# Optimization experiments

Measured on AMD Instinct MI355X. Metric: run time of the kernel, lower is better.

## Reference

```python
import jax, jax.numpy as jnp
import numpy as np

SEM_DIM = 512
SEM_SIZE = 2048
N_LEVELS = 9           # acoustic FSQ levels
HALF = (N_LEVELS - 1) / 2.0
EPS = 1e-5


def setup_inputs() -> dict:
    key = jax.random.key(0)
    k1, k2, k3, k4, k5, k6 = jax.random.split(key, 6)
    B, T, ACO_DIM = 16, 4096, 32
    return {
        "x": jax.random.normal(k1, (B, SEM_DIM + ACO_DIM, T), dtype=jnp.float32),
        "embedding_sum": jax.random.normal(k2, (SEM_SIZE, SEM_DIM), dtype=jnp.float32),
        "cluster_usage": jax.random.uniform(k3, (SEM_SIZE,), dtype=jnp.float32),
        "noise": jax.random.uniform(k4, (B, ACO_DIM, T), dtype=jnp.float32),
        "probs_sem": jax.random.uniform(k5, (B,), dtype=jnp.float32),
        "probs_aco": jax.random.uniform(k6, (B,), dtype=jnp.float32),
    }


def reference(x, embedding_sum, cluster_usage, noise, probs_sem, probs_aco):
    sem_in = x[:, :SEM_DIM, :]          # [B, 512, T]
    aco_in = x[:, SEM_DIM:, :]          # [B, 32, T]
    B, D, T = sem_in.shape

    # ---- semantic VQ path (cdist + argmin + embedding lookup + STE) ----
    emb = embedding_sum / jnp.clip(cluster_usage, EPS, None)[:, None]  # [K, D]
    xf = sem_in.transpose(0, 2, 1).reshape(B * T, D)                   # (b t) d
    # squared euclidean distance (argmin identical to cdist p=2 argmin)
    d2 = (jnp.sum(xf * xf, axis=1, keepdims=True)
          - 2.0 * (xf @ emb.T)
          + jnp.sum(emb * emb, axis=1))                                # [BT, K]
    sem_codes = jnp.argmin(d2, axis=-1).reshape(B, 1, T)               # [B,1,T]
    sem_quant = emb[sem_codes[:, 0, :]].transpose(0, 2, 1)             # b d t
    sem_mask = (probs_sem < 0.5)[:, None, None]
    sem_ste = sem_in + jax.lax.stop_gradient(sem_quant - sem_in)
    sem_out = jnp.where(sem_mask, sem_ste, sem_in)

    # ---- acoustic FSQ path with 50/25/25 stochastic routing ----
    z_b = jnp.tanh(aco_in) * HALF
    z_q = z_b + jax.lax.stop_gradient(jnp.round(z_b) - z_b)            # round STE
    noise_s = (noise * 2.0 - 1.0) * (1.0 / N_LEVELS) * HALF            # U[-s, s]*half
    z_dither = jnp.clip(z_b + noise_s, -HALF, HALF)
    qm = (probs_aco < 0.5)[:, None, None]
    dm = ((probs_aco >= 0.5) & (probs_aco < 0.75))[:, None, None]
    z_out = jnp.where(qm, z_q, jnp.where(dm, z_dither, z_b))
    aco_codes = jnp.clip(jnp.round(z_out + HALF), 0, N_LEVELS - 1).astype(jnp.int32)
    z_norm = z_out / HALF

    quantized = jnp.concatenate([sem_out, z_norm], axis=1)             # [B,544,T]
    codes = jnp.concatenate([sem_codes.astype(jnp.int32), aco_codes], axis=1)
    return quantized, codes
```

## Files before the change

kernel.cpp:

```cpp
#include <hip/hip_runtime.h>
#include <math.h>
#include <stdint.h>

typedef _Float16 f16;
typedef _Float16 f16x8 __attribute__((ext_vector_type(8)));
typedef float f32x4 __attribute__((ext_vector_type(4)));

#define B_    16
#define T_    4096
#define SEM   512
#define ACO   32
#define XROWS 544
#define CODES 2048
#define EPSC  1e-5f
#define HALFC 4.0f
#define ECLAMP 60000.0f


__global__ void bias_kernel(const float* __restrict__ esum,
                            const float* __restrict__ usage,
                            float* __restrict__ bias) {
    int c = blockIdx.x;
    float u = fmaxf(usage[c], EPSC);
    float s = 0.f;
    for (int d = threadIdx.x; d < SEM; d += 64) {
        float v = esum[(size_t)c * SEM + d] / u;
        s += v * v;
    }
    for (int off = 32; off; off >>= 1) s += __shfl_down(s, off);
    if (threadIdx.x == 0) bias[c] = 0.5f * s;
}

__global__ void embT_kernel(const float* __restrict__ esum,
                            const float* __restrict__ usage,
                            float* __restrict__ embT) {
    __shared__ float tile[32][33];
    int c0 = blockIdx.x * 32;
    int d0 = blockIdx.y * 32;
    int col = threadIdx.x & 31, r = threadIdx.x >> 5;
    for (int i = r; i < 32; i += 8) {
        float u = fmaxf(usage[c0 + i], EPSC);
        tile[col][i] = esum[(size_t)(c0 + i) * SEM + d0 + col] / u;
    }
    __syncthreads();
    for (int i = r; i < 32; i += 8)
        embT[(size_t)(d0 + i) * CODES + c0 + col] = tile[i][col];
}

__global__ void esplit_kernel(const float* __restrict__ esum,
                              const float* __restrict__ usage,
                              f16* __restrict__ EhT, f16* __restrict__ ElT) {
    int c = blockIdx.x;
    float u = fmaxf(usage[c], EPSC);
    for (int d = threadIdx.x; d < SEM; d += 256) {
        float e = esum[(size_t)c * SEM + d] / u;
        e = fminf(fmaxf(e, -ECLAMP), ECLAMP);
        f16 h = (f16)e;
        EhT[(size_t)c * SEM + d] = h;
        ElT[(size_t)c * SEM + d] = (f16)(e - (float)h);
    }
}

__global__ void xsplit_kernel(const float* __restrict__ x,
                              f16* __restrict__ XhT, f16* __restrict__ XlT) {
    int m0 = blockIdx.x * 256;
    int d0 = blockIdx.y * 32;
    int b  = m0 >> 12;
    int t  = (m0 & 4095) + (int)threadIdx.x;
    const float* xp = x + ((size_t)b * XROWS + d0) * T_ + t;
    int m = m0 + (int)threadIdx.x;

    f16x8 hv[4], lv[4];
#pragma unroll
    for (int j = 0; j < 4; j++) {
#pragma unroll
        for (int e = 0; e < 8; e++) {
            float v = xp[(size_t)(j * 8 + e) * T_];
            f16 h = (f16)v;
            hv[j][e] = h;
            lv[j][e] = (f16)(v - (float)h);
        }
    }
    f16* oh = XhT + (size_t)m * SEM + d0;
    f16* ol = XlT + (size_t)m * SEM + d0;
#pragma unroll
    for (int j = 0; j < 4; j++) {
        *(f16x8*)(oh + j * 8) = hv[j];
        *(f16x8*)(ol + j * 8) = lv[j];
    }
}

#define MB 256
#define NQ 512
#define NC 128
#define BK 32

__device__ __forceinline__ void gl_lds16(const f16* g, f16* l) {
    __builtin_amdgcn_global_load_lds(
        (const __attribute__((address_space(1))) unsigned int*)(g),
        (__attribute__((address_space(3))) unsigned int*)(l),
        16, 0, 0);
}

__global__ __launch_bounds__(256, 2) void argmin_mfma(
        const f16* __restrict__ XhT, const f16* __restrict__ XlT,
        const f16* __restrict__ EhT, const f16* __restrict__ ElT,
        const float* __restrict__ bias,
        float* __restrict__ pScore, int* __restrict__ pIdx) {
    __shared__ __align__(16) f16 Xh[MB * BK];
    __shared__ __align__(16) f16 Xl[MB * BK];
    __shared__ __align__(16) f16 Eh[NC * BK];
    __shared__ __align__(16) f16 El[NC * BK];

    int tid = threadIdx.x;
    int w   = tid >> 6;
    int l   = tid & 63;
    int q   = l >> 4;
    int r16 = l & 15;

    int m0      = blockIdx.x * MB;
    int quarter = blockIdx.y;

    int aoff = (w * 64 + r16) * BK + q * 8;
    int boff = r16 * BK + q * 8;

    float bestS[16];
    int   bestI[16];
#pragma unroll
    for (int i = 0; i < 16; i++) { bestS[i] = -3.4e38f; bestI[i] = 0; }

    for (int nc = 0; nc < 4; nc++) {
        int nbase = quarter * NQ + nc * NC;
        float bb[8];
#pragma unroll
        for (int ni = 0; ni < 8; ni++) bb[ni] = bias[nbase + ni * 16 + r16];

        f32x4 acc[4][8];
#pragma unroll
        for (int mi = 0; mi < 4; mi++)
#pragma unroll
            for (int ni = 0; ni < 8; ni++)
                acc[mi][ni] = (f32x4){0.f, 0.f, 0.f, 0.f};

        for (int k0 = 0; k0 < SEM; k0 += BK) {
            __syncthreads();
#pragma unroll
            for (int ii = 0; ii < 4; ii++) {
                int off16 = ii * 256 + tid;
                int mm = off16 >> 2, ch = off16 & 3;
                int gsrc = (m0 + mm) * SEM + k0 + ch * 8;
                gl_lds16(XhT + gsrc, Xh + off16 * 8);
                gl_lds16(XlT + gsrc, Xl + off16 * 8);
            }
#pragma unroll
            for (int ii = 0; ii < 2; ii++) {
                int off16 = ii * 256 + tid;
                int nn = off16 >> 2, ch = off16 & 3;
                int gsrc = (nbase + nn) * SEM + k0 + ch * 8;
                gl_lds16(EhT + gsrc, Eh + off16 * 8);
                gl_lds16(ElT + gsrc, El + off16 * 8);
            }
            __syncthreads();

            f16x8 ah[4], al[4];
#pragma unroll
            for (int mi = 0; mi < 4; mi++) {
                ah[mi] = *(const f16x8*)&Xh[aoff + mi * 16 * BK];
                al[mi] = *(const f16x8*)&Xl[aoff + mi * 16 * BK];
            }
#pragma unroll
            for (int ni = 0; ni < 8; ni++) {
                f16x8 bh = *(const f16x8*)&Eh[boff + ni * 16 * BK];
                f16x8 bl = *(const f16x8*)&El[boff + ni * 16 * BK];
#pragma unroll
                for (int mi = 0; mi < 4; mi++) {
                    f32x4 a0 = acc[mi][ni];
                    a0 = __builtin_amdgcn_mfma_f32_16x16x32_f16(al[mi], bh, a0, 0, 0, 0);
                    a0 = __builtin_amdgcn_mfma_f32_16x16x32_f16(ah[mi], bl, a0, 0, 0, 0);
                    a0 = __builtin_amdgcn_mfma_f32_16x16x32_f16(ah[mi], bh, a0, 0, 0, 0);
                    acc[mi][ni] = a0;
                }
            }
        }
#pragma unroll
        for (int ni = 0; ni < 8; ni++) {
            int n = nbase + ni * 16 + r16;
#pragma unroll
            for (int mi = 0; mi < 4; mi++)
#pragma unroll
                for (int reg = 0; reg < 4; reg++) {
                    float s = acc[mi][ni][reg] - bb[ni];
                    int slot = mi * 4 + reg;
                    if (s > bestS[slot]) { bestS[slot] = s; bestI[slot] = n; }
                }
        }
    }

#pragma unroll
    for (int mask = 1; mask < 16; mask <<= 1) {
#pragma unroll
        for (int slot = 0; slot < 16; slot++) {
            float os = __shfl_xor(bestS[slot], mask);
            int   oi = __shfl_xor(bestI[slot], mask);
            if (os > bestS[slot] || (os == bestS[slot] && oi < bestI[slot])) {
                bestS[slot] = os; bestI[slot] = oi;
            }
        }
    }
    if (r16 == 0) {
#pragma unroll
        for (int mi = 0; mi < 4; mi++)
#pragma unroll
            for (int reg = 0; reg < 4; reg++) {
                int m = m0 + w * 64 + mi * 16 + q * 4 + reg;
                pScore[quarter * 65536 + m] = bestS[mi * 4 + reg];
                pIdx  [quarter * 65536 + m] = bestI[mi * 4 + reg];
            }
    }
}

__global__ void merge_kernel(const float* __restrict__ pScore,
                             const int* __restrict__ pIdx,
                             int* __restrict__ codesW,
                             float* __restrict__ codes_out) {
    int m = blockIdx.x * 256 + threadIdx.x;
    float bs = pScore[m]; int bi = pIdx[m];
    for (int qq = 1; qq < 4; qq++) {
        float s = pScore[qq * 65536 + m];
        int  ii = pIdx[qq * 65536 + m];
        if (s > bs || (s == bs && ii < bi)) { bs = s; bi = ii; }
    }
    codesW[m] = bi;
    int bb2 = m >> 12, t = m & 4095;
    codes_out[(size_t)bb2 * 33 * T_ + t] = (float)bi;
}

__global__ void finalize_kernel(const float* __restrict__ x,
                                const float* __restrict__ embT,
                                const int* __restrict__ codes_ws,
                                const float* __restrict__ noise,
                                const float* __restrict__ probs_sem,
                                const float* __restrict__ probs_aco,
                                float* __restrict__ out,
                                float* __restrict__ codes_out) {
    const size_t N0 = (size_t)B_ * SEM * T_;
    const size_t N1 = (size_t)B_ * ACO * T_;
    size_t idx = (size_t)blockIdx.x * 256 + threadIdx.x;
    if (idx < N0) {
        int t = (int)(idx & 4095);
        int d = (int)((idx >> 12) & 511);
        int b = (int)(idx >> 21);
        float v;
        if (probs_sem[b] < 0.5f) {
            int c = codes_ws[(b << 12) + t];
            v = embT[(size_t)d * CODES + c];
        } else {
            v = x[((size_t)(b * XROWS + d)) * T_ + t];
        }
        out[((size_t)(b * XROWS + d)) * T_ + t] = v;
    } else if (idx < N0 + N1) {
        size_t i2 = idx - N0;
        int t = (int)(i2 & 4095);
        int j = (int)((i2 >> 12) & 31);
        int b = (int)(i2 >> 17);
        float a  = x[((size_t)(b * XROWS + SEM + j)) * T_ + t];
        float zb = tanhf(a) * HALFC;
        float p  = probs_aco[b];
        float zo;
        if (p < 0.5f) {
            zo = rintf(zb);
        } else if (p < 0.75f) {
            float nz = noise[((size_t)(b * ACO + j)) * T_ + t];
            float ns = ((nz * 2.0f - 1.0f) * (float)(1.0 / 9.0)) * HALFC;
            zo = fminf(fmaxf(zb + ns, -HALFC), HALFC);
        } else {
            zo = zb;
        }
        float code = fminf(fmaxf(rintf(zo + HALFC), 0.f), 8.f);
        out[((size_t)(b * XROWS + SEM + j)) * T_ + t] = zo * 0.25f;
        codes_out[((size_t)(b * 33 + 1 + j)) * T_ + t] = code;
    }
}

extern "C" void kernel_launch(void* const* d_in, const int* in_sizes, int n_in,
                              void* d_out, int out_size, void* d_ws, size_t ws_size,
                              hipStream_t stream) {
    const float* x      = (const float*)d_in[0];
    const float* esum   = (const float*)d_in[1];
    const float* usage  = (const float*)d_in[2];
    const float* noise  = (const float*)d_in[3];
    const float* psem   = (const float*)d_in[4];
    const float* paco   = (const float*)d_in[5];
    float* out = (float*)d_out;

    float* wsf    = (float*)d_ws;
    float* embT   = wsf;
    float* bias   = wsf + 1048576;
    int*   codesW = (int*)(wsf + 1050624);
    f16*   EhT    = (f16*)(wsf + 1116160);
    f16*   ElT    = (f16*)(wsf + 1640448);
    float* pScore = wsf + 2164736;
    int*   pIdx   = (int*)(wsf + 2426880);

    const size_t QOFF = (size_t)B_ * XROWS * T_;
    float* codes_out = out + QOFF;

    f16* XhT = (f16*)out;
    f16* XlT = (f16*)(out + 16777216);

    xsplit_kernel<<<dim3((B_ * T_) / 256, SEM / 32), 256, 0, stream>>>(x, XhT, XlT);
    bias_kernel<<<CODES, 64, 0, stream>>>(esum, usage, bias);
    embT_kernel<<<dim3(CODES / 32, SEM / 32), 256, 0, stream>>>(esum, usage, embT);
    esplit_kernel<<<CODES, 256, 0, stream>>>(esum, usage, EhT, ElT);
    argmin_mfma<<<dim3((B_ * T_) / MB, 4), 256, 0, stream>>>(XhT, XlT, EhT, ElT,
                                                             bias, pScore, pIdx);
    merge_kernel<<<(B_ * T_) / 256, 256, 0, stream>>>(pScore, pIdx, codesW, codes_out);
    const size_t NTOT = (size_t)B_ * SEM * T_ + (size_t)B_ * ACO * T_;
    finalize_kernel<<<(int)(NTOT / 256), 256, 0, stream>>>(x, embT, codesW, noise,
                                                           psem, paco, out, codes_out);
}
```

Baseline: 828.8 us.

## Double-buffer argmin GEMM over full codebook and fuse merge into kernel

The argmin kernel now has 512 threads in a 2x4 wave layout, each block covering all 2048 codes with 256-code chunks. A double-buffered LDS pipeline prefetches the next K-slice while MFMAs run on the current one. The separate per-quarter partial-score buffers and the merge kernel are dropped, with the two column-waves' results reduced through shared memory. The cost is fewer blocks (256 instead of 1024), 128KB of LDS per block that can limit occupancy, and one barrier per K-step.

```diff
diff --git a/kernel.cpp b/kernel.cpp
--- a/kernel.cpp
+++ b/kernel.cpp
@@ -90,10 +90,14 @@
     }
 }
 
-#define MB 256
-#define NQ 512
-#define NC 128
-#define BK 32
+#define MB   256
+#define NCB  256
+#define BK   32
+#define NTH  512
+#define NCHN (CODES / NCB)
+#define KT   (SEM / BK)
+#define PL   8192
+#define BUF  32768
 
 __device__ __forceinline__ void gl_lds16(const f16* g, f16* l) {
     __builtin_amdgcn_global_load_lds(
@@ -102,98 +106,105 @@
         16, 0, 0);
 }
 
-__global__ __launch_bounds__(256, 2) void argmin_mfma(
+__global__ __launch_bounds__(NTH, 2) void argmin_mfma(
         const f16* __restrict__ XhT, const f16* __restrict__ XlT,
         const f16* __restrict__ EhT, const f16* __restrict__ ElT,
         const float* __restrict__ bias,
-        float* __restrict__ pScore, int* __restrict__ pIdx) {
-    __shared__ __align__(16) f16 Xh[MB * BK];
-    __shared__ __align__(16) f16 Xl[MB * BK];
-    __shared__ __align__(16) f16 Eh[NC * BK];
-    __shared__ __align__(16) f16 El[NC * BK];
+        int* __restrict__ codesW, float* __restrict__ codes_out) {
+    __shared__ __align__(16) f16 smem[2 * BUF];
 
     int tid = threadIdx.x;
     int w   = tid >> 6;
     int l   = tid & 63;
     int q   = l >> 4;
     int r16 = l & 15;
-
-    int m0      = blockIdx.x * MB;
-    int quarter = blockIdx.y;
-
-    int aoff = (w * 64 + r16) * BK + q * 8;
-    int boff = r16 * BK + q * 8;
+    int wm  = w >> 1;
+    int wn  = w & 1;
+
+    int m0 = blockIdx.x * MB;
+
+    int sr = tid >> 2;
+    int sc = (tid & 3) * 8;
 
     float bestS[16];
     int   bestI[16];
 #pragma unroll
     for (int i = 0; i < 16; i++) { bestS[i] = -3.4e38f; bestI[i] = 0; }
 
-    for (int nc = 0; nc < 4; nc++) {
-        int nbase = quarter * NQ + nc * NC;
-        float bb[8];
-#pragma unroll
-        for (int ni = 0; ni < 8; ni++) bb[ni] = bias[nbase + ni * 16 + r16];
-
-        f32x4 acc[4][8];
-#pragma unroll
-        for (int mi = 0; mi < 4; mi++)
-#pragma unroll
-            for (int ni = 0; ni < 8; ni++)
-                acc[mi][ni] = (f32x4){0.f, 0.f, 0.f, 0.f};
-
-        for (int k0 = 0; k0 < SEM; k0 += BK) {
-            __syncthreads();
-#pragma unroll
-            for (int ii = 0; ii < 4; ii++) {
-                int off16 = ii * 256 + tid;
-                int mm = off16 >> 2, ch = off16 & 3;
-                int gsrc = (m0 + mm) * SEM + k0 + ch * 8;
-                gl_lds16(XhT + gsrc, Xh + off16 * 8);
-                gl_lds16(XlT + gsrc, Xl + off16 * 8);
-            }
-#pragma unroll
-            for (int ii = 0; ii < 2; ii++) {
-                int off16 = ii * 256 + tid;
-                int nn = off16 >> 2, ch = off16 & 3;
-                int gsrc = (nbase + nn) * SEM + k0 + ch * 8;
-                gl_lds16(EhT + gsrc, Eh + off16 * 8);
-                gl_lds16(ElT + gsrc, El + off16 * 8);
-            }
-            __syncthreads();
-
-            f16x8 ah[4], al[4];
+    f32x4 acc[4][8];
+#pragma unroll
+    for (int mi = 0; mi < 4; mi++)
+#pragma unroll
+        for (int ni = 0; ni < 8; ni++)
+            acc[mi][ni] = (f32x4){0.f, 0.f, 0.f, 0.f};
+
+#define STAGE(BI, NB, KK) do {                                              \
+    f16* sb = smem + (BI) * BUF;                                            \
+    _Pragma("unroll")                                                       \
+    for (int ii = 0; ii < 8; ii++) {                                        \
+        int rr = (ii & 1) * 128 + sr;                                       \
+        int ldsOff = (ii >> 1) * PL + rr * 32 + sc;                         \
+        const f16* g;                                                       \
+        if ((ii >> 1) == 0)      g = XhT + (size_t)(m0 + rr) * SEM + (KK) + sc; \
+        else if ((ii >> 1) == 1) g = XlT + (size_t)(m0 + rr) * SEM + (KK) + sc; \
+        else if ((ii >> 1) == 2) g = EhT + (size_t)((NB) + rr) * SEM + (KK) + sc; \
+        else                     g = ElT + (size_t)((NB) + rr) * SEM + (KK) + sc; \
+        gl_lds16(g, sb + ldsOff);                                           \
+    }                                                                       \
+} while (0)
+
+    STAGE(0, 0, 0);
+    __syncthreads();
+
+    for (int t = 0; t < NCHN * KT; t++) {
+        int cur   = t & 1;
+        int nbase = (t >> 4) * NCB;
+
+        if (t + 1 < NCHN * KT) {
+            int t1 = t + 1;
+            STAGE(cur ^ 1, (t1 >> 4) * NCB, (t1 & 15) * BK);
+        }
+
+        const f16* bp = smem + cur * BUF;
+        f16x8 ah[4], al[4];
+#pragma unroll
+        for (int mi = 0; mi < 4; mi++) {
+            int ao = (wm * 64 + mi * 16 + r16) * 32 + q * 8;
+            ah[mi] = *(const f16x8*)&bp[ao];
+            al[mi] = *(const f16x8*)&bp[ao + PL];
+        }
+#pragma unroll
+        for (int ni = 0; ni < 8; ni++) {
+            int bo = 2 * PL + (wn * 128 + ni * 16 + r16) * 32 + q * 8;
+            f16x8 bh = *(const f16x8*)&bp[bo];
+            f16x8 bl = *(const f16x8*)&bp[bo + PL];
 #pragma unroll
             for (int mi = 0; mi < 4; mi++) {
-                ah[mi] = *(const f16x8*)&Xh[aoff + mi * 16 * BK];
-                al[mi] = *(const f16x8*)&Xl[aoff + mi * 16 * BK];
-            }
+                f32x4 a0 = acc[mi][ni];
+                a0 = __builtin_amdgcn_mfma_f32_16x16x32_f16(al[mi], bh, a0, 0, 0, 0);
+                a0 = __builtin_amdgcn_mfma_f32_16x16x32_f16(ah[mi], bl, a0, 0, 0, 0);
+                a0 = __builtin_amdgcn_mfma_f32_16x16x32_f16(ah[mi], bh, a0, 0, 0, 0);
+                acc[mi][ni] = a0;
+            }
+        }
+
+        if ((t & 15) == 15) {
 #pragma unroll
             for (int ni = 0; ni < 8; ni++) {
-                f16x8 bh = *(const f16x8*)&Eh[boff + ni * 16 * BK];
-                f16x8 bl = *(const f16x8*)&El[boff + ni * 16 * BK];
-#pragma unroll
-                for (int mi = 0; mi < 4; mi++) {
-                    f32x4 a0 = acc[mi][ni];
-                    a0 = __builtin_amdgcn_mfma_f32_16x16x32_f16(al[mi], bh, a0, 0, 0, 0);
-                    a0 = __builtin_amdgcn_mfma_f32_16x16x32_f16(ah[mi], bl, a0, 0, 0, 0);
-                    a0 = __builtin_amdgcn_mfma_f32_16x16x32_f16(ah[mi], bh, a0, 0, 0, 0);
-                    acc[mi][ni] = a0;
-                }
-            }
-        }
-#pragma unroll
-        for (int ni = 0; ni < 8; ni++) {
-            int n = nbase + ni * 16 + r16;
-#pragma unroll
-            for (int mi = 0; mi < 4; mi++)
-#pragma unroll
-                for (int reg = 0; reg < 4; reg++) {
-                    float s = acc[mi][ni][reg] - bb[ni];
-                    int slot = mi * 4 + reg;
-                    if (s > bestS[slot]) { bestS[slot] = s; bestI[slot] = n; }
-                }
-        }
+                int n = nbase + wn * 128 + ni * 16 + r16;
+                float bb = bias[n];
+#pragma unroll
+                for (int mi = 0; mi < 4; mi++)
+#pragma unroll
+                    for (int reg = 0; reg < 4; reg++) {
+                        float s = acc[mi][ni][reg] - bb;
+                        int slot = mi * 4 + reg;
+                        if (s > bestS[slot]) { bestS[slot] = s; bestI[slot] = n; }
+                        acc[mi][ni][reg] = 0.f;
+                    }
+            }
+        }
+        __syncthreads();
     }
 
 #pragma unroll
@@ -207,32 +218,42 @@
             }
         }
     }
-    if (r16 == 0) {
-#pragma unroll
-        for (int mi = 0; mi < 4; mi++)
-#pragma unroll
-            for (int reg = 0; reg < 4; reg++) {
-                int m = m0 + w * 64 + mi * 16 + q * 4 + reg;
-                pScore[quarter * 65536 + m] = bestS[mi * 4 + reg];
-                pIdx  [quarter * 65536 + m] = bestI[mi * 4 + reg];
-            }
-    }
-}
-
-__global__ void merge_kernel(const float* __restrict__ pScore,
-                             const int* __restrict__ pIdx,
-                             int* __restrict__ codesW,
-                             float* __restrict__ codes_out) {
-    int m = blockIdx.x * 256 + threadIdx.x;
-    float bs = pScore[m]; int bi = pIdx[m];
-    for (int qq = 1; qq < 4; qq++) {
-        float s = pScore[qq * 65536 + m];
-        int  ii = pIdx[qq * 65536 + m];
-        if (s > bs || (s == bs && ii < bi)) { bs = s; bi = ii; }
-    }
-    codesW[m] = bi;
-    int bb2 = m >> 12, t = m & 4095;
-    codes_out[(size_t)bb2 * 33 * T_ + t] = (float)bi;
+
+    {
+        float* sMS = (float*)smem;
+        int*   sMI = (int*)(sMS + 8 * 4 * 16);
+        if (r16 == 0) {
+            int base = (w * 4 + q) * 16;
+#pragma unroll
+            for (int slot = 0; slot < 16; slot++) {
+                sMS[base + slot] = bestS[slot];
+                sMI[base + slot] = bestI[slot];
+            }
+        }
+        __syncthreads();
+        if (wn == 0 && r16 == 0) {
+            int pbase = ((w + 1) * 4 + q) * 16;
+#pragma unroll
+            for (int slot = 0; slot < 16; slot++) {
+                float os = sMS[pbase + slot];
+                int   oi = sMI[pbase + slot];
+                if (os > bestS[slot] || (os == bestS[slot] && oi < bestI[slot])) {
+                    bestS[slot] = os; bestI[slot] = oi;
+                }
+            }
+#pragma unroll
+            for (int mi = 0; mi < 4; mi++)
+#pragma unroll
+                for (int reg = 0; reg < 4; reg++) {
+                    int m = m0 + wm * 64 + mi * 16 + q * 4 + reg;
+                    int bi = bestI[mi * 4 + reg];
+                    codesW[m] = bi;
+                    int bb2 = m >> 12, tt = m & 4095;
+                    codes_out[(size_t)bb2 * 33 * T_ + tt] = (float)bi;
+                }
+        }
+    }
+#undef STAGE
 }
 
 __global__ void finalize_kernel(const float* __restrict__ x,
@@ -299,8 +320,6 @@
     int*   codesW = (int*)(wsf + 1050624);
     f16*   EhT    = (f16*)(wsf + 1116160);
     f16*   ElT    = (f16*)(wsf + 1640448);
-    float* pScore = wsf + 2164736;
-    int*   pIdx   = (int*)(wsf + 2426880);
 
     const size_t QOFF = (size_t)B_ * XROWS * T_;
     float* codes_out = out + QOFF;
@@ -312,9 +331,8 @@
     bias_kernel<<<CODES, 64, 0, stream>>>(esum, usage, bias);
     embT_kernel<<<dim3(CODES / 32, SEM / 32), 256, 0, stream>>>(esum, usage, embT);
     esplit_kernel<<<CODES, 256, 0, stream>>>(esum, usage, EhT, ElT);
-    argmin_mfma<<<dim3((B_ * T_) / MB, 4), 256, 0, stream>>>(XhT, XlT, EhT, ElT,
-                                                             bias, pScore, pIdx);
-    merge_kernel<<<(B_ * T_) / 256, 256, 0, stream>>>(pScore, pIdx, codesW, codes_out);
+    argmin_mfma<<<(B_ * T_) / MB, NTH, 0, stream>>>(XhT, XlT, EhT, ElT, bias,
+                                                    codesW, codes_out);
     const size_t NTOT = (size_t)B_ * SEM * T_ + (size_t)B_ * ACO * T_;
     finalize_kernel<<<(int)(NTOT / 256), 256, 0, stream>>>(x, embT, codesW, noise,
                                                            psem, paco, out, codes_out);
```

Measured after the change: 719.3 us. 13.2% less time.
